# Kernel tuning notes

Hardware: AMD Instinct MI355X
Metric: run time of the kernel (lower is better)

## Reference

```python
import jax, jax.numpy as jnp
import numpy as np

B, S, R = 1, 128, 384          # batch, n_seq (MSA rows), n_res
C_M, C_Z, H, D = 256, 128, 8, 32  # msa channels, pair channels, heads, head dim


def layernorm(x, g, b, eps=1e-5):
    mu = jnp.mean(x, axis=-1, keepdims=True)
    var = jnp.var(x, axis=-1, keepdims=True)
    return (x - mu) * jax.lax.rsqrt(var + eps) * g + b


def setup_inputs() -> dict:
    key = jax.random.key(0)
    ks = jax.random.split(key, 10)
    w = lambda k, shape: jax.random.normal(k, shape, jnp.float32) * 0.02
    return {
        "msa_act": jax.random.normal(ks[0], (B, S, R, C_M), jnp.float32),
        "pair_act": jax.random.normal(ks[1], (B, R, R, C_Z), jnp.float32),
        "msa_mask": jnp.ones((B, S, R), jnp.float32),
        "qn_g": jnp.ones((C_M,), jnp.float32),
        "qn_b": jnp.zeros((C_M,), jnp.float32),
        "pn_g": jnp.ones((C_Z,), jnp.float32),
        "pn_b": jnp.zeros((C_Z,), jnp.float32),
        "w_pair": w(ks[2], (C_Z, H)),           # feat_2d_weights (no bias)
        "wq": w(ks[3], (C_M, H, D)),
        "wk": w(ks[4], (C_M, H, D)),
        "wv": w(ks[5], (C_M, H, D)),
        "wg": w(ks[6], (C_M, H, D)),            # gating linear
        "bg": jnp.ones((H, D), jnp.float32),     # gating bias (AF2 inits to 1)
        "wo": w(ks[7], (H, D, C_M)),             # output projection
        "bo": jnp.zeros((C_M,), jnp.float32),
    }


def reference(msa_act, pair_act, msa_mask, qn_g, qn_b, pn_g, pn_b,
              w_pair, wq, wk, wv, wg, bg, wo, bo):
    # pair bias: LN + Linear(c_z -> H), -> [B, 1, H, R, R]
    z = jnp.einsum('bijc,ch->bhij', layernorm(pair_act, pn_g, pn_b), w_pair)[:, None]
    # mask bias: [B, S, 1, 1, R]
    mask_bias = (1e9 * (msa_mask - 1.0))[:, :, None, None, :]

    m = layernorm(msa_act, qn_g, qn_b)
    q = jnp.einsum('bsrc,chd->bshrd', m, wq) * (D ** -0.5)
    k = jnp.einsum('bsrc,chd->bshrd', m, wk)
    v = jnp.einsum('bsrc,chd->bshrd', m, wv)

    logits = jnp.einsum('bshqd,bshkd->bshqk', q, k) + mask_bias + z  # [B,S,H,R,R]
    a = jax.nn.softmax(logits, axis=-1)
    o = jnp.einsum('bshqk,bshkd->bsqhd', a, v)                       # [B,S,R,H,D]

    g = jax.nn.sigmoid(jnp.einsum('bsrc,chd->bsrhd', m, wg) + bg)
    out = jnp.einsum('bsrhd,hdc->bsrc', o * g, wo) + bo              # [B,S,R,C_M]
    return out
```

## Files before the change

### kernel.cpp

```cpp
#include <hip/hip_runtime.h>
#include <hip/hip_bf16.h>

typedef unsigned int uint;
typedef unsigned short ushortT;
typedef __attribute__((ext_vector_type(8))) short bf16x8;
typedef __attribute__((ext_vector_type(4))) float f32x4;

#define S_ 128
#define R_ 384
#define CM 256
#define CZ 128
#define H_ 8
#define D_ 32
#define SR (S_*R_)
#define RRTOT (R_*R_)
#define SHRD (S_*H_*R_*D_)

__device__ __forceinline__ float bf2f(ushortT u) {
    return __uint_as_float(((uint)u) << 16);
}
__device__ __forceinline__ ushortT f2bf(float f) {
    uint x = __float_as_uint(f);
    x += 0x7FFFu + ((x >> 16) & 1u);
    return (ushortT)(x >> 16);
}
__device__ __forceinline__ uint pack_bf2(float lo, float hi) {
    return (uint)f2bf(lo) | ((uint)f2bf(hi) << 16);
}

__global__ __launch_bounds__(256) void k_prep(
        const float* __restrict__ wq, const float* __restrict__ wk,
        const float* __restrict__ wv, const float* __restrict__ wg,
        const float* __restrict__ wo,
        ushortT* __restrict__ wt, ushortT* __restrict__ wgt,
        ushortT* __restrict__ wot) {
    int id = blockIdx.x * 256 + threadIdx.x;
    int which = id >> 16, r16 = id & 65535;
    int y = r16 & 255, x = r16 >> 8;
    if (which == 0)      wt[(size_t)y*256 + x]       = f2bf(wq[(size_t)x*256 + y] * 0.17677669529663687f);
    else if (which == 1) wt[(size_t)(256+y)*256 + x] = f2bf(wk[(size_t)x*256 + y]);
    else if (which == 2) wt[(size_t)(512+y)*256 + x] = f2bf(wv[(size_t)x*256 + y]);
    else if (which == 3) wgt[(size_t)y*256 + x]      = f2bf(wg[(size_t)x*256 + y]);
    else                 wot[(size_t)y*256 + x]      = f2bf(wo[(size_t)x*256 + y]);
}

__global__ __launch_bounds__(256) void k_pair_bias(
        const float* __restrict__ pair, const float* __restrict__ pn_g,
        const float* __restrict__ pn_b, const float* __restrict__ w_pair,
        ushortT* __restrict__ z) {
    int wave = threadIdx.x >> 6, lane = threadIdx.x & 63;
    int row = blockIdx.x * 4 + wave;
    const float* x = pair + (size_t)row * CZ;
    float x0 = x[lane], x1 = x[lane + 64];
    float s = x0 + x1;
    #pragma unroll
    for (int off = 32; off; off >>= 1) s += __shfl_xor(s, off);
    float mu = s * (1.0f / 128.0f);
    float e0 = x0 - mu, e1 = x1 - mu;
    float v2 = e0*e0 + e1*e1;
    #pragma unroll
    for (int off = 32; off; off >>= 1) v2 += __shfl_xor(v2, off);
    float rstd = rsqrtf(v2 * (1.0f / 128.0f) + 1e-5f);
    float n0 = e0 * rstd * pn_g[lane]      + pn_b[lane];
    float n1 = e1 * rstd * pn_g[lane + 64] + pn_b[lane + 64];
    float res[8];
    #pragma unroll
    for (int h = 0; h < 8; ++h) {
        float p = n0 * w_pair[lane*8 + h] + n1 * w_pair[(lane+64)*8 + h];
        #pragma unroll
        for (int off = 32; off; off >>= 1) p += __shfl_xor(p, off);
        res[h] = p;
    }
    #pragma unroll
    for (int h = 0; h < 8; ++h)
        if (lane == h) z[(size_t)h * RRTOT + row] = f2bf(res[h]);
}

__device__ __forceinline__ void ln_row_f4(
        const float* __restrict__ src, const float* __restrict__ gam,
        const float* __restrict__ bet, char* msb, int row, int lane) {
    float4 xv = *(const float4*)&src[lane * 4];
    float sm = (xv.x + xv.y) + (xv.z + xv.w);
    #pragma unroll
    for (int off = 32; off; off >>= 1) sm += __shfl_xor(sm, off);
    float mu = sm * (1.0f / 256.0f);
    float e0 = xv.x - mu, e1 = xv.y - mu, e2 = xv.z - mu, e3 = xv.w - mu;
    float vv = (e0*e0 + e1*e1) + (e2*e2 + e3*e3);
    #pragma unroll
    for (int off = 32; off; off >>= 1) vv += __shfl_xor(vv, off);
    float rstd = rsqrtf(vv * (1.0f / 256.0f) + 1e-5f);
    float4 gv = *(const float4*)&gam[lane * 4];
    float4 bv = *(const float4*)&bet[lane * 4];
    float n0 = e0 * rstd * gv.x + bv.x, n1 = e1 * rstd * gv.y + bv.y;
    float n2 = e2 * rstd * gv.z + bv.z, n3 = e3 * rstd * gv.w + bv.w;
    uint2 w; w.x = pack_bf2(n0, n1); w.y = pack_bf2(n2, n3);
    *(uint2*)(msb + ((row*512 + lane*8) ^ ((row & 7) << 4))) = w;
}

__global__ __launch_bounds__(256, 4) void k_msa_qkv(
        const float* __restrict__ msa, const float* __restrict__ qn_g,
        const float* __restrict__ qn_b, const ushortT* __restrict__ wt,
        ushortT* __restrict__ qo, ushortT* __restrict__ ko,
        ushortT* __restrict__ vto) {
    __shared__ ushortT m_sh[32 * 256];
    int tid = threadIdx.x, wave = tid >> 6, lane = tid & 63;
    int c = lane & 15, g = (lane >> 4) & 3;
    int r0 = blockIdx.x * 32, s = r0 / R_, rl0 = r0 % R_;
    char* msb = (char*)m_sh;

    #pragma unroll
    for (int i = 0; i < 8; ++i) {
        int row = wave * 8 + i;
        ln_row_f4(msa + (size_t)(r0 + row) * CM, qn_g, qn_b, msb, row, lane);
    }
    __syncthreads();

    bf16x8 af[2][8];
    #pragma unroll
    for (int rt = 0; rt < 2; ++rt)
        #pragma unroll
        for (int kc = 0; kc < 8; ++kc) {
            int row = rt*16 + c;
            af[rt][kc] = *(const bf16x8*)(msb + ((row*512 + (kc*32 + 8*g)*2) ^ ((c & 7) << 4)));
        }

    const f32x4 z4 = {0.f, 0.f, 0.f, 0.f};
    #pragma unroll
    for (int kk = 0; kk < 6; ++kk) {
        int tb = wave * 2 + kk * 8;
        int ctA = tb, ctB = tb + 1;
        const ushortT* wbA = wt + ((size_t)((ctA >> 4)*256 + (ctA & 15)*16 + c)) * 256 + 8*g;
        const ushortT* wbB = wt + ((size_t)((ctB >> 4)*256 + (ctB & 15)*16 + c)) * 256 + 8*g;
        f32x4 aA0 = z4, aA1 = z4, aB0 = z4, aB1 = z4;
        #pragma unroll
        for (int kc = 0; kc < 8; ++kc) {
            bf16x8 b0 = *(const bf16x8*)(wbA + kc*32);
            bf16x8 b1 = *(const bf16x8*)(wbB + kc*32);
            aA0 = __builtin_amdgcn_mfma_f32_16x16x32_bf16(af[0][kc], b0, aA0, 0, 0, 0);
            aA1 = __builtin_amdgcn_mfma_f32_16x16x32_bf16(af[1][kc], b0, aA1, 0, 0, 0);
            aB0 = __builtin_amdgcn_mfma_f32_16x16x32_bf16(af[0][kc], b1, aB0, 0, 0, 0);
            aB1 = __builtin_amdgcn_mfma_f32_16x16x32_bf16(af[1][kc], b1, aB1, 0, 0, 0);
        }
        #pragma unroll
        for (int j = 0; j < 2; ++j) {
            int ct = tb + j;
            int mI = ct >> 4, t0 = (ct & 15) * 16, hh = t0 >> 5, d0 = t0 & 31;
            size_t hb = (size_t)(s * H_ + hh);
            f32x4 v0 = j ? aB0 : aA0;
            f32x4 v1 = j ? aB1 : aA1;
            #pragma unroll
            for (int r = 0; r < 4; ++r) {
                int rl = rl0 + 4*g + r;
                ushortT vv = f2bf(v0[r]);
                if (mI == 0)      qo[(hb * R_ + rl) * D_ + d0 + c] = vv;
                else if (mI == 1) ko[(hb * R_ + rl) * D_ + d0 + c] = vv;
                else              vto[(hb * D_ + d0 + c) * R_ + rl] = vv;
            }
            #pragma unroll
            for (int r = 0; r < 4; ++r) {
                int rl = rl0 + 16 + 4*g + r;
                ushortT vv = f2bf(v1[r]);
                if (mI == 0)      qo[(hb * R_ + rl) * D_ + d0 + c] = vv;
                else if (mI == 1) ko[(hb * R_ + rl) * D_ + d0 + c] = vv;
                else              vto[(hb * D_ + d0 + c) * R_ + rl] = vv;
            }
        }
    }
}

__global__ __launch_bounds__(512) void k_attn(
        const ushortT* __restrict__ qws, const ushortT* __restrict__ kws,
        const ushortT* __restrict__ vtws, const ushortT* __restrict__ zws,
        const float* __restrict__ mask, float* __restrict__ out) {
    __shared__ ushortT k_sh[R_ * 40];
    __shared__ ushortT vt_sh[D_ * R_];
    __shared__ float   mb[R_];
    __shared__ ushortT p_sh[8 * 1280];
    int tid = threadIdx.x, wave = tid >> 6, lane = tid & 63;
    int c = lane & 15, g = (lane >> 4) & 3;
    int s = blockIdx.x >> 3, h = blockIdx.x & 7;
    size_t base = (size_t)(s * H_ + h) * R_ * D_;

    {
        const uint4* ks = (const uint4*)(kws + base);
        char* kb_ = (char*)k_sh;
        for (int i = tid; i < 1536; i += 512) {
            int row = i >> 2, part = i & 3;
            *(uint4*)(kb_ + row*80 + part*16) = ks[i];
        }
        const uint4* vs = (const uint4*)(vtws + base);
        char* vb = (char*)vt_sh;
        for (int i = tid; i < 1536; i += 512) {
            int d = i / 48, ch = i % 48;
            *(uint4*)(vb + ((d*768 + ch*16) ^ ((d & 7) << 4))) = vs[i];
        }
        for (int j = tid; j < R_; j += 512) mb[j] = 1e9f * (mask[s*R_ + j] - 1.0f);
    }
    __syncthreads();

    const char* ksb = (const char*)k_sh;
    const char* vtb = (const char*)vt_sh;
    char* psb = (char*)p_sh + wave * 2560;
    const f32x4 zero4 = {0.f, 0.f, 0.f, 0.f};

    for (int qt = wave; qt < 24; qt += 8) {
        int q0 = qt * 16;
        bf16x8 qf = *(const bf16x8*)(qws + base + (size_t)(q0 + c) * D_ + 8*g);
        const ushortT* zq = zws + (size_t)h * RRTOT + (size_t)(q0 + c) * R_ + 4*g;

        float sm = 0.f;
        f32x4 o0 = zero4, o1 = zero4;
        #pragma unroll 2
        for (int kb = 0; kb < 12; ++kb) {
            bf16x8 kfA = *(const bf16x8*)(ksb + ((2*kb    )*16 + c)*80 + 16*g);
            bf16x8 kfB = *(const bf16x8*)(ksb + ((2*kb + 1)*16 + c)*80 + 16*g);
            f32x4 pA = __builtin_amdgcn_mfma_f32_16x16x32_bf16(kfA, qf, zero4, 0, 0, 0);
            f32x4 pB = __builtin_amdgcn_mfma_f32_16x16x32_bf16(kfB, qf, zero4, 0, 0, 0);
            float4 mvA = *(const float4*)&mb[(2*kb    )*16 + 4*g];
            float4 mvB = *(const float4*)&mb[(2*kb + 1)*16 + 4*g];
            ushort4 zvA = *(const ushort4*)(zq + (2*kb    )*16);
            ushort4 zvB = *(const ushort4*)(zq + (2*kb + 1)*16);
            pA.x = __expf(pA.x + mvA.x + bf2f(zvA.x));
            pA.y = __expf(pA.y + mvA.y + bf2f(zvA.y));
            pA.z = __expf(pA.z + mvA.z + bf2f(zvA.z));
            pA.w = __expf(pA.w + mvA.w + bf2f(zvA.w));
            pB.x = __expf(pB.x + mvB.x + bf2f(zvB.x));
            pB.y = __expf(pB.y + mvB.y + bf2f(zvB.y));
            pB.z = __expf(pB.z + mvB.z + bf2f(zvB.z));
            pB.w = __expf(pB.w + mvB.w + bf2f(zvB.w));
            sm += (pA.x + pA.y) + (pA.z + pA.w) + (pB.x + pB.y) + (pB.z + pB.w);
            uint2 wA; wA.x = pack_bf2(pA.x, pA.y); wA.y = pack_bf2(pA.z, pA.w);
            uint2 wB; wB.x = pack_bf2(pB.x, pB.y); wB.y = pack_bf2(pB.z, pB.w);
            *(uint2*)(psb + (kb&1)*1280 + c*80 +      8*g) = wA;
            *(uint2*)(psb + (kb&1)*1280 + c*80 + 32 + 8*g) = wB;
            bf16x8 pa = *(const bf16x8*)(psb + (kb&1)*1280 + c*80 + 16*g);
            bf16x8 v0 = *(const bf16x8*)(vtb + (((c     )*768 + kb*64 + 16*g) ^ ((c & 7) << 4)));
            bf16x8 v1 = *(const bf16x8*)(vtb + (((16 + c)*768 + kb*64 + 16*g) ^ ((c & 7) << 4)));
            o0 = __builtin_amdgcn_mfma_f32_16x16x32_bf16(v0, pa, o0, 0, 0, 0);
            o1 = __builtin_amdgcn_mfma_f32_16x16x32_bf16(v1, pa, o1, 0, 0, 0);
        }
        sm += __shfl_xor(sm, 16);
        sm += __shfl_xor(sm, 32);
        float inv = 1.0f / sm;
        float4 s0, s1;
        s0.x = o0[0]*inv; s0.y = o0[1]*inv; s0.z = o0[2]*inv; s0.w = o0[3]*inv;
        s1.x = o1[0]*inv; s1.y = o1[1]*inv; s1.z = o1[2]*inv; s1.w = o1[3]*inv;
        float* ob = out + (size_t)(s*R_ + q0 + c) * CM + h*D_ + 4*g;
        *(float4*)ob = s0;
        *(float4*)(ob + 16) = s1;
    }
}

__global__ __launch_bounds__(256, 4) void k_out(
        const float* __restrict__ msa, const float* __restrict__ qn_g,
        const float* __restrict__ qn_b, const ushortT* __restrict__ wgt,
        const float* __restrict__ bg, const ushortT* __restrict__ wot,
        const float* __restrict__ bo, float* __restrict__ out) {
    __shared__ ushortT m_sh[32 * 256];
    __shared__ ushortT og_sh[32 * 256];
    int tid = threadIdx.x, wave = tid >> 6, lane = tid & 63;
    int c = lane & 15, g = (lane >> 4) & 3;
    int r0 = blockIdx.x * 32;
    char* msb = (char*)m_sh;
    char* ogb = (char*)og_sh;

    #pragma unroll
    for (int i = 0; i < 8; ++i) {
        int row = wave * 8 + i;
        ln_row_f4(msa + (size_t)(r0 + row) * CM, qn_g, qn_b, msb, row, lane);
    }
    __syncthreads();

    bf16x8 af[2][8];
    #pragma unroll
    for (int rt = 0; rt < 2; ++rt)
        #pragma unroll
        for (int kc = 0; kc < 8; ++kc) {
            int row = rt*16 + c;
            af[rt][kc] = *(const bf16x8*)(msb + ((row*512 + (kc*32 + 8*g)*2) ^ ((c & 7) << 4)));
        }

    const f32x4 z4 = {0.f, 0.f, 0.f, 0.f};
    #pragma unroll
    for (int kk = 0; kk < 2; ++kk) {
        int tb = wave * 2 + kk * 8;
        const ushortT* wbA = wgt + (size_t)(tb*16 + c) * 256 + 8*g;
        const ushortT* wbB = wgt + (size_t)((tb+1)*16 + c) * 256 + 8*g;
        f32x4 aA0 = z4, aA1 = z4, aB0 = z4, aB1 = z4;
        #pragma unroll
        for (int kc = 0; kc < 8; ++kc) {
            bf16x8 b0 = *(const bf16x8*)(wbA + kc*32);
            bf16x8 b1 = *(const bf16x8*)(wbB + kc*32);
            aA0 = __builtin_amdgcn_mfma_f32_16x16x32_bf16(af[0][kc], b0, aA0, 0, 0, 0);
            aA1 = __builtin_amdgcn_mfma_f32_16x16x32_bf16(af[1][kc], b0, aA1, 0, 0, 0);
            aB0 = __builtin_amdgcn_mfma_f32_16x16x32_bf16(af[0][kc], b1, aB0, 0, 0, 0);
            aB1 = __builtin_amdgcn_mfma_f32_16x16x32_bf16(af[1][kc], b1, aB1, 0, 0, 0);
        }
        #pragma unroll
        for (int j = 0; j < 2; ++j) {
            int t = (tb + j)*16 + c;
            float bgv = bg[t];
            f32x4 v0 = j ? aB0 : aA0;
            f32x4 v1 = j ? aB1 : aA1;
            #pragma unroll
            for (int rt = 0; rt < 2; ++rt) {
                f32x4 vr = rt ? v1 : v0;
                #pragma unroll
                for (int r = 0; r < 4; ++r) {
                    int row = rt*16 + 4*g + r;
                    float gv = 1.0f / (1.0f + __expf(-(vr[r] + bgv)));
                    float ov = out[(size_t)(r0 + row) * CM + t];
                    *(ushortT*)(ogb + ((row*512 + t*2) ^ ((row & 7) << 4))) = f2bf(ov * gv);
                }
            }
        }
    }
    __syncthreads();

    bf16x8 af2[2][8];
    #pragma unroll
    for (int rt = 0; rt < 2; ++rt)
        #pragma unroll
        for (int kc = 0; kc < 8; ++kc) {
            int row = rt*16 + c;
            af2[rt][kc] = *(const bf16x8*)(ogb + ((row*512 + (kc*32 + 8*g)*2) ^ ((c & 7) << 4)));
        }

    #pragma unroll
    for (int kk = 0; kk < 2; ++kk) {
        int tb = wave * 2 + kk * 8;
        const ushortT* wbA = wot + (size_t)(tb*16 + c) * 256 + 8*g;
        const ushortT* wbB = wot + (size_t)((tb+1)*16 + c) * 256 + 8*g;
        f32x4 aA0 = z4, aA1 = z4, aB0 = z4, aB1 = z4;
        #pragma unroll
        for (int kc = 0; kc < 8; ++kc) {
            bf16x8 b0 = *(const bf16x8*)(wbA + kc*32);
            bf16x8 b1 = *(const bf16x8*)(wbB + kc*32);
            aA0 = __builtin_amdgcn_mfma_f32_16x16x32_bf16(af2[0][kc], b0, aA0, 0, 0, 0);
            aA1 = __builtin_amdgcn_mfma_f32_16x16x32_bf16(af2[1][kc], b0, aA1, 0, 0, 0);
            aB0 = __builtin_amdgcn_mfma_f32_16x16x32_bf16(af2[0][kc], b1, aB0, 0, 0, 0);
            aB1 = __builtin_amdgcn_mfma_f32_16x16x32_bf16(af2[1][kc], b1, aB1, 0, 0, 0);
        }
        #pragma unroll
        for (int j = 0; j < 2; ++j) {
            int t = (tb + j)*16 + c;
            float bov = bo[t];
            f32x4 v0 = j ? aB0 : aA0;
            f32x4 v1 = j ? aB1 : aA1;
            #pragma unroll
            for (int rt = 0; rt < 2; ++rt) {
                f32x4 vr = rt ? v1 : v0;
                #pragma unroll
                for (int r = 0; r < 4; ++r)
                    out[(size_t)(r0 + rt*16 + 4*g + r) * CM + t] = vr[r] + bov;
            }
        }
    }
}

extern "C" void kernel_launch(void* const* d_in, const int* in_sizes, int n_in,
                              void* d_out, int out_size, void* d_ws, size_t ws_size,
                              hipStream_t stream) {
    const float* msa    = (const float*)d_in[0];
    const float* pair   = (const float*)d_in[1];
    const float* mask   = (const float*)d_in[2];
    const float* qn_g   = (const float*)d_in[3];
    const float* qn_b   = (const float*)d_in[4];
    const float* pn_g   = (const float*)d_in[5];
    const float* pn_b   = (const float*)d_in[6];
    const float* w_pair = (const float*)d_in[7];
    const float* wq     = (const float*)d_in[8];
    const float* wk     = (const float*)d_in[9];
    const float* wv     = (const float*)d_in[10];
    const float* wg     = (const float*)d_in[11];
    const float* bg     = (const float*)d_in[12];
    const float* wo     = (const float*)d_in[13];
    const float* bo     = (const float*)d_in[14];
    float* out = (float*)d_out;

    ushortT* qws  = (ushortT*)d_ws;
    ushortT* kws  = qws + (size_t)SHRD;
    ushortT* vtws = kws + (size_t)SHRD;
    ushortT* zws  = vtws + (size_t)SHRD;
    ushortT* wt   = zws + (size_t)H_ * RRTOT;
    ushortT* wgt  = wt + 3 * 65536;
    ushortT* wot  = wgt + 65536;

    k_prep     <<<1280,    256, 0, stream>>>(wq, wk, wv, wg, wo, wt, wgt, wot);
    k_pair_bias<<<RRTOT/4, 256, 0, stream>>>(pair, pn_g, pn_b, w_pair, zws);
    k_msa_qkv  <<<SR/32,   256, 0, stream>>>(msa, qn_g, qn_b, wt, qws, kws, vtws);
    k_attn     <<<S_*H_,   512, 0, stream>>>(qws, kws, vtws, zws, mask, out);
    k_out      <<<SR/32,   256, 0, stream>>>(msa, qn_g, qn_b, wgt, bg, wot, bo, out);
}
```

Baseline: 329.1 us.

## Stage QKV outputs through LDS for coalesced 16-byte stores; vectorize pair-bias reduction

The QKV projection kernel now writes each MFMA result tile into a swizzled shared-memory buffer and then stores Q, K and transposed V to global memory with coalesced 16-byte writes, replacing scattered 2-byte stores. This adds two barriers per projection and an extra 16 KB of LDS, and drops the occupancy hint from launch bounds. The pair-bias kernel switches to vectorized loads, a single-pass mean and variance, and a butterfly shuffle reduction that computes all 8 heads at once instead of 8 separate full reductions.

```diff
diff --git a/kernel.cpp b/kernel.cpp
--- a/kernel.cpp
+++ b/kernel.cpp
@@ -51,29 +51,48 @@
     int wave = threadIdx.x >> 6, lane = threadIdx.x & 63;
     int row = blockIdx.x * 4 + wave;
     const float* x = pair + (size_t)row * CZ;
-    float x0 = x[lane], x1 = x[lane + 64];
-    float s = x0 + x1;
-    #pragma unroll
-    for (int off = 32; off; off >>= 1) s += __shfl_xor(s, off);
-    float mu = s * (1.0f / 128.0f);
-    float e0 = x0 - mu, e1 = x1 - mu;
-    float v2 = e0*e0 + e1*e1;
-    #pragma unroll
-    for (int off = 32; off; off >>= 1) v2 += __shfl_xor(v2, off);
-    float rstd = rsqrtf(v2 * (1.0f / 128.0f) + 1e-5f);
-    float n0 = e0 * rstd * pn_g[lane]      + pn_b[lane];
-    float n1 = e1 * rstd * pn_g[lane + 64] + pn_b[lane + 64];
-    float res[8];
-    #pragma unroll
-    for (int h = 0; h < 8; ++h) {
-        float p = n0 * w_pair[lane*8 + h] + n1 * w_pair[(lane+64)*8 + h];
-        #pragma unroll
-        for (int off = 32; off; off >>= 1) p += __shfl_xor(p, off);
-        res[h] = p;
-    }
-    #pragma unroll
-    for (int h = 0; h < 8; ++h)
-        if (lane == h) z[(size_t)h * RRTOT + row] = f2bf(res[h]);
+    float2 xv = *(const float2*)&x[lane * 2];
+    float s  = xv.x + xv.y;
+    float s2 = xv.x*xv.x + xv.y*xv.y;
+    #pragma unroll
+    for (int off = 32; off; off >>= 1) {
+        s  += __shfl_xor(s,  off);
+        s2 += __shfl_xor(s2, off);
+    }
+    float mu  = s * (1.0f / 128.0f);
+    float var = s2 * (1.0f / 128.0f) - mu * mu;
+    float rstd = rsqrtf(var + 1e-5f);
+    float2 gv = *(const float2*)&pn_g[lane * 2];
+    float2 bv = *(const float2*)&pn_b[lane * 2];
+    float n0 = (xv.x - mu) * rstd * gv.x + bv.x;
+    float n1 = (xv.y - mu) * rstd * gv.y + bv.y;
+    float4 wa = *(const float4*)&w_pair[lane*16     ];
+    float4 wb = *(const float4*)&w_pair[lane*16 +  4];
+    float4 wc = *(const float4*)&w_pair[lane*16 +  8];
+    float4 wd = *(const float4*)&w_pair[lane*16 + 12];
+    float v0_ = n0*wa.x + n1*wc.x, v1_ = n0*wa.y + n1*wc.y;
+    float v2_ = n0*wa.z + n1*wc.z, v3_ = n0*wa.w + n1*wc.w;
+    float v4_ = n0*wb.x + n1*wd.x, v5_ = n0*wb.y + n1*wd.y;
+    float v6_ = n0*wb.z + n1*wd.z, v7_ = n0*wb.w + n1*wd.w;
+    float x0 = __shfl_xor(v0_,1), x1 = __shfl_xor(v1_,1), x2 = __shfl_xor(v2_,1), x3 = __shfl_xor(v3_,1);
+    float x4 = __shfl_xor(v4_,1), x5 = __shfl_xor(v5_,1), x6 = __shfl_xor(v6_,1), x7 = __shfl_xor(v7_,1);
+    bool b0 = (lane & 1) != 0;
+    float u0 = b0 ? v4_+x4 : v0_+x0;
+    float u1 = b0 ? v5_+x5 : v1_+x1;
+    float u2 = b0 ? v6_+x6 : v2_+x2;
+    float u3 = b0 ? v7_+x7 : v3_+x3;
+    float y0 = __shfl_xor(u0,2), y1 = __shfl_xor(u1,2), y2 = __shfl_xor(u2,2), y3 = __shfl_xor(u3,2);
+    bool b1 = (lane & 2) != 0;
+    float w0 = b1 ? u2+y2 : u0+y0;
+    float w1 = b1 ? u3+y3 : u1+y1;
+    float z0 = __shfl_xor(w0,4), z1 = __shfl_xor(w1,4);
+    bool b2 = (lane & 4) != 0;
+    float val = b2 ? w1+z1 : w0+z0;
+    val += __shfl_xor(val, 8);
+    val += __shfl_xor(val, 16);
+    val += __shfl_xor(val, 32);
+    int hmap = 4*(lane & 1) + 2*((lane >> 1) & 1) + ((lane >> 2) & 1);
+    if (lane < 8) z[(size_t)hmap * RRTOT + row] = f2bf(val);
 }
 
 __device__ __forceinline__ void ln_row_f4(
@@ -97,16 +116,18 @@
     *(uint2*)(msb + ((row*512 + lane*8) ^ ((row & 7) << 4))) = w;
 }
 
-__global__ __launch_bounds__(256, 4) void k_msa_qkv(
+__global__ __launch_bounds__(256) void k_msa_qkv(
         const float* __restrict__ msa, const float* __restrict__ qn_g,
         const float* __restrict__ qn_b, const ushortT* __restrict__ wt,
         ushortT* __restrict__ qo, ushortT* __restrict__ ko,
         ushortT* __restrict__ vto) {
     __shared__ ushortT m_sh[32 * 256];
+    __shared__ ushortT o_sh[32 * 256];
     int tid = threadIdx.x, wave = tid >> 6, lane = tid & 63;
     int c = lane & 15, g = (lane >> 4) & 3;
     int r0 = blockIdx.x * 32, s = r0 / R_, rl0 = r0 % R_;
     char* msb = (char*)m_sh;
+    char* osb = (char*)o_sh;
 
     #pragma unroll
     for (int i = 0; i < 8; ++i) {
@@ -125,46 +146,67 @@
         }
 
     const f32x4 z4 = {0.f, 0.f, 0.f, 0.f};
-    #pragma unroll
-    for (int kk = 0; kk < 6; ++kk) {
-        int tb = wave * 2 + kk * 8;
-        int ctA = tb, ctB = tb + 1;
-        const ushortT* wbA = wt + ((size_t)((ctA >> 4)*256 + (ctA & 15)*16 + c)) * 256 + 8*g;
-        const ushortT* wbB = wt + ((size_t)((ctB >> 4)*256 + (ctB & 15)*16 + c)) * 256 + 8*g;
-        f32x4 aA0 = z4, aA1 = z4, aB0 = z4, aB1 = z4;
-        #pragma unroll
-        for (int kc = 0; kc < 8; ++kc) {
-            bf16x8 b0 = *(const bf16x8*)(wbA + kc*32);
-            bf16x8 b1 = *(const bf16x8*)(wbB + kc*32);
-            aA0 = __builtin_amdgcn_mfma_f32_16x16x32_bf16(af[0][kc], b0, aA0, 0, 0, 0);
-            aA1 = __builtin_amdgcn_mfma_f32_16x16x32_bf16(af[1][kc], b0, aA1, 0, 0, 0);
-            aB0 = __builtin_amdgcn_mfma_f32_16x16x32_bf16(af[0][kc], b1, aB0, 0, 0, 0);
-            aB1 = __builtin_amdgcn_mfma_f32_16x16x32_bf16(af[1][kc], b1, aB1, 0, 0, 0);
-        }
-        #pragma unroll
-        for (int j = 0; j < 2; ++j) {
-            int ct = tb + j;
-            int mI = ct >> 4, t0 = (ct & 15) * 16, hh = t0 >> 5, d0 = t0 & 31;
-            size_t hb = (size_t)(s * H_ + hh);
-            f32x4 v0 = j ? aB0 : aA0;
-            f32x4 v1 = j ? aB1 : aA1;
+    for (int mI = 0; mI < 3; ++mI) {
+        #pragma unroll
+        for (int kk = 0; kk < 2; ++kk) {
+            int tb = wave * 2 + kk * 8;
+            const ushortT* wbA = wt + ((size_t)(mI*256 + tb*16 + c)) * 256 + 8*g;
+            const ushortT* wbB = wbA + 16 * 256;
+            f32x4 aA0 = z4, aA1 = z4, aB0 = z4, aB1 = z4;
             #pragma unroll
-            for (int r = 0; r < 4; ++r) {
-                int rl = rl0 + 4*g + r;
-                ushortT vv = f2bf(v0[r]);
-                if (mI == 0)      qo[(hb * R_ + rl) * D_ + d0 + c] = vv;
-                else if (mI == 1) ko[(hb * R_ + rl) * D_ + d0 + c] = vv;
-                else              vto[(hb * D_ + d0 + c) * R_ + rl] = vv;
-            }
+            for (int kc = 0; kc < 8; ++kc) {
+                bf16x8 b0 = *(const bf16x8*)(wbA + kc*32);
+                bf16x8 b1 = *(const bf16x8*)(wbB + kc*32);
+                aA0 = __builtin_amdgcn_mfma_f32_16x16x32_bf16(af[0][kc], b0, aA0, 0, 0, 0);
+                aA1 = __builtin_amdgcn_mfma_f32_16x16x32_bf16(af[1][kc], b0, aA1, 0, 0, 0);
+                aB0 = __builtin_amdgcn_mfma_f32_16x16x32_bf16(af[0][kc], b1, aB0, 0, 0, 0);
+                aB1 = __builtin_amdgcn_mfma_f32_16x16x32_bf16(af[1][kc], b1, aB1, 0, 0, 0);
+            }
+            if (mI < 2) {
+                #pragma unroll
+                for (int r = 0; r < 4; ++r) {
+                    int row0 = 4*g + r, row1 = 16 + 4*g + r;
+                    int colA = tb*16 + c, colB = colA + 16;
+                    *(ushortT*)(osb + ((row0*512 + colA*2) ^ ((row0 & 7) << 4))) = f2bf(aA0[r]);
+                    *(ushortT*)(osb + ((row1*512 + colA*2) ^ ((row1 & 7) << 4))) = f2bf(aA1[r]);
+                    *(ushortT*)(osb + ((row0*512 + colB*2) ^ ((row0 & 7) << 4))) = f2bf(aB0[r]);
+                    *(ushortT*)(osb + ((row1*512 + colB*2) ^ ((row1 & 7) << 4))) = f2bf(aB1[r]);
+                }
+            } else {
+                #pragma unroll
+                for (int r = 0; r < 4; ++r) {
+                    int rlo = 4*g + r, rhi = 16 + 4*g + r;
+                    int hdA = tb*16 + c, hdB = hdA + 16;
+                    *(ushortT*)(osb + ((hdA*64 + rlo*2) ^ ((hdA & 3) << 4))) = f2bf(aA0[r]);
+                    *(ushortT*)(osb + ((hdA*64 + rhi*2) ^ ((hdA & 3) << 4))) = f2bf(aA1[r]);
+                    *(ushortT*)(osb + ((hdB*64 + rlo*2) ^ ((hdB & 3) << 4))) = f2bf(aB0[r]);
+                    *(ushortT*)(osb + ((hdB*64 + rhi*2) ^ ((hdB & 3) << 4))) = f2bf(aB1[r]);
+                }
+            }
+        }
+        __syncthreads();
+        if (mI < 2) {
+            ushortT* O = (mI == 0) ? qo : ko;
             #pragma unroll
-            for (int r = 0; r < 4; ++r) {
-                int rl = rl0 + 16 + 4*g + r;
-                ushortT vv = f2bf(v1[r]);
-                if (mI == 0)      qo[(hb * R_ + rl) * D_ + d0 + c] = vv;
-                else if (mI == 1) ko[(hb * R_ + rl) * D_ + d0 + c] = vv;
-                else              vto[(hb * D_ + d0 + c) * R_ + rl] = vv;
-            }
-        }
+            for (int i = 0; i < 4; ++i) {
+                int idx = tid + i*256;
+                int row = idx >> 5, c16 = idx & 31;
+                uint4 vd = *(const uint4*)(osb + ((row*512 + c16*16) ^ ((row & 7) << 4)));
+                int hh = c16 >> 2, dq = (c16 & 3) * 8;
+                size_t ga = ((size_t)(s*H_ + hh) * R_ + rl0 + row) * D_ + dq;
+                *(uint4*)&O[ga] = vd;
+            }
+        } else {
+            #pragma unroll
+            for (int i = 0; i < 4; ++i) {
+                int idx = tid + i*256;
+                int hd = idx >> 2, q8 = idx & 3;
+                uint4 vd = *(const uint4*)(osb + ((hd*64 + q8*16) ^ ((hd & 3) << 4)));
+                size_t ga = ((size_t)(s*256 + hd)) * R_ + rl0 + q8*8;
+                *(uint4*)&vto[ga] = vd;
+            }
+        }
+        __syncthreads();
     }
 }
 
```

Result: faster. 278.9 us (-15.2%).
